# Performance work log

Hardware: AMD Instinct MI355X
Metric: run time of the kernel (lower is better)

The kernel has to match this reference:

```python
import jax, jax.numpy as jnp
import numpy as np

H = 16          # num_heads
K = 15          # kernel_size (padding_l = K-1, causal)
EPS = 1e-5      # LayerNorm eps


def setup_inputs() -> dict:
    key = jax.random.key(0)
    ks = jax.random.split(key, 8)
    T, B, C, F = 1024, 8, 1024, 4096
    n = lambda k, shape, scale=1.0: jax.random.normal(k, shape, jnp.float32) * scale
    return {
        "x": n(ks[0], (T, B, C)),
        "w_lin": n(ks[1], (C, H * K), 0.02),      # dynamic-conv weight projection
        "b_lin": jnp.zeros((H * K,), jnp.float32),
        "ln_g": jnp.ones((C,), jnp.float32),
        "ln_b": jnp.zeros((C,), jnp.float32),
        "fc1_w": n(ks[2], (C, F), 0.02),
        "fc1_b": jnp.zeros((F,), jnp.float32),
        "fc2_w": n(ks[3], (F, C), 0.02),
        "fc2_b": jnp.zeros((C,), jnp.float32),
    }


def _dynamic_conv(x, w_lin, b_lin):
    # x: (T, B, C). Per-timestep weights -> softmax over kernel -> causal conv.
    T, B, C = x.shape
    R = C // H  # channels per head
    w = jnp.einsum('tbc,ck->tbk', x, w_lin) + b_lin          # (T, B, H*K)
    w = jax.nn.softmax(w.reshape(T, B, H, K), axis=-1)        # softmax over kernel taps
    # causal left-padding: tap k sees x[t + k - (K-1)]
    xp = jnp.pad(x, ((K - 1, 0), (0, 0), (0, 0))).reshape(T + K - 1, B, H, R)
    o = jnp.zeros((T, B, H, R), x.dtype)
    for k in range(K):  # fixed small kernel loop; avoids (T,B,C,K) unfold tensor
        o = o + w[:, :, :, k:k + 1] * xp[k:k + T]
    return o.reshape(T, B, C)


def _layer_norm(y, g, b):
    mu = jnp.mean(y, axis=-1, keepdims=True)
    var = jnp.var(y, axis=-1, keepdims=True)
    return (y - mu) * jax.lax.rsqrt(var + EPS) * g + b


def _forward(x, w_lin, b_lin, ln_g, ln_b, fc1_w, fc1_b, fc2_w, fc2_b):
    y = _dynamic_conv(x, w_lin, b_lin)
    y = _layer_norm(y, ln_g, ln_b)
    h = jax.nn.relu(jnp.einsum('tbc,cf->tbf', y, fc1_w) + fc1_b)
    out = jnp.einsum('tbf,fc->tbc', h, fc2_w) + fc2_b
    return out + y  # residual around FFN (residual taken post-LayerNorm)


def reference(x, w_lin, b_lin, ln_g, ln_b, fc1_w, fc1_b, fc2_w, fc2_b):
    return _forward(x, w_lin, b_lin, ln_g, ln_b, fc1_w, fc1_b, fc2_w, fc2_b)
```

## Files before the change

### kernel.cpp

```cpp
#include <hip/hip_runtime.h>


#define T_DIM 1024
#define B_DIM 8
#define C_DIM 1024
#define F_DIM 4096
#define H_DIM 16
#define K_TAP 15
#define TB (T_DIM * B_DIM)

typedef __attribute__((ext_vector_type(8))) short short8;
typedef __attribute__((ext_vector_type(4))) float f32x4;

__device__ __forceinline__ float bf2f(unsigned short u) {
    union { unsigned int i; float f; } v; v.i = ((unsigned int)u) << 16; return v.f;
}
__device__ __forceinline__ unsigned short f2bf(float f) {
    union { float f; unsigned int i; } v; v.f = f;
    unsigned int r = v.i + 0x7fffu + ((v.i >> 16) & 1u);
    return (unsigned short)(r >> 16);
}

__device__ __forceinline__ void async_copy16(const void* gptr, void* lptr) {
    __builtin_amdgcn_global_load_lds(
        (const __attribute__((address_space(1))) void*)gptr,
        (__attribute__((address_space(3))) void*)lptr, 16, 0, 0);
}

__global__ void cvt_bf16(const float* __restrict__ in, unsigned short* __restrict__ out) {
    int i = (blockIdx.x * 256 + threadIdx.x) * 4;
    float4 v = *(const float4*)(in + i);
    unsigned short a = f2bf(v.x), b = f2bf(v.y), c = f2bf(v.z), d = f2bf(v.w);
    uint2 o;
    o.x = (unsigned int)a | ((unsigned int)b << 16);
    o.y = (unsigned int)c | ((unsigned int)d << 16);
    *(uint2*)(out + i) = o;
}

__global__ void transpose_pad(const float* __restrict__ in,
                              unsigned short* __restrict__ out,
                              int R, int Cin, int Cpad) {
    __shared__ unsigned short tile[32][33];
    const int c0 = blockIdx.x * 32, r0 = blockIdx.y * 32;
    const int x = threadIdx.x, y = threadIdx.y;
#pragma unroll
    for (int j = 0; j < 4; j++) {
        int r = r0 + y + j * 8, c = c0 + x;
        unsigned short v = 0;
        if (c < Cin) v = f2bf(in[(size_t)r * Cin + c]);
        tile[y + j * 8][x] = v;
    }
    __syncthreads();
#pragma unroll
    for (int j = 0; j < 4; j++) {
        out[(size_t)(c0 + y + j * 8) * R + (r0 + x)] = tile[x][y + j * 8];
    }
}

template <int MODE>
__global__ __launch_bounds__(256)
void gemm_bt(const unsigned short* __restrict__ A,
             const unsigned short* __restrict__ Bt,
             void* __restrict__ Cout_v,
             int M, int N, int K, int kz,
             const float* __restrict__ bias,
             const unsigned short* __restrict__ resid) {
    __shared__ __align__(16) unsigned short As[2][128 * 32];
    __shared__ __align__(16) unsigned short Bs[2][128 * 32];

    const int tid = threadIdx.x;
    const int m0 = blockIdx.y * 128;
    const int n0 = blockIdx.x * 128;
    const int kbase = blockIdx.z * kz;
    const int wave = tid >> 6, lane = tid & 63;
    const int quad = lane >> 4, l16 = lane & 15;
    const int wm = (wave >> 1) * 64;
    const int wn = (wave & 1) * 64;

    f32x4 acc[4][4];
#pragma unroll
    for (int i = 0; i < 4; i++)
#pragma unroll
        for (int j = 0; j < 4; j++) acc[i][j] = (f32x4){0.f, 0.f, 0.f, 0.f};

    const int r_local = lane >> 2;
    const int kc_g = (lane & 3) ^ ((lane >> 3) & 3);
    const unsigned short* gA0 = A + (size_t)(m0 + wave * 32 + r_local) * K + kbase + kc_g * 8;
    const unsigned short* gA1 = gA0 + (size_t)16 * K;
    const unsigned short* gB0 = Bt + (size_t)(n0 + wave * 32 + r_local) * K + kbase + kc_g * 8;
    const unsigned short* gB1 = gB0 + (size_t)16 * K;
    unsigned short* lA[2] = {&As[0][wave * 32 * 32], &As[1][wave * 32 * 32]};
    unsigned short* lB[2] = {&Bs[0][wave * 32 * 32], &Bs[1][wave * 32 * 32]};

    const int xorsw = (l16 >> 1) & 3;

    async_copy16(gA0, lA[0]);
    async_copy16(gA1, lA[0] + 16 * 32);
    async_copy16(gB0, lB[0]);
    async_copy16(gB1, lB[0] + 16 * 32);

    int buf = 0;
    for (int k0 = 0; k0 < kz; k0 += 32) {
        __syncthreads();

        const int nk = k0 + 32;
        if (nk < kz) {
            const int nb = buf ^ 1;
            async_copy16(gA0 + nk, lA[nb]);
            async_copy16(gA1 + nk, lA[nb] + 16 * 32);
            async_copy16(gB0 + nk, lB[nb]);
            async_copy16(gB1 + nk, lB[nb] + 16 * 32);
        }

        short8 af[4], bfr[4];
#pragma unroll
        for (int i = 0; i < 4; i++) {
            af[i]  = *(const short8*)(&As[buf][(wm + i * 16 + l16) * 32 + (quad ^ xorsw) * 8]);
            bfr[i] = *(const short8*)(&Bs[buf][(wn + i * 16 + l16) * 32 + (quad ^ xorsw) * 8]);
        }
#pragma unroll
        for (int mi = 0; mi < 4; mi++)
#pragma unroll
            for (int nj = 0; nj < 4; nj++)
                acc[mi][nj] = __builtin_amdgcn_mfma_f32_16x16x32_bf16(
                    af[mi], bfr[nj], acc[mi][nj], 0, 0, 0);
        buf ^= 1;
    }

    const int crow0 = m0 + wm + quad * 4;
    const int ccol0 = n0 + wn + l16;
    if (MODE == 3) {
        float* Cf = (float*)Cout_v + (size_t)blockIdx.z * M * N;
#pragma unroll
        for (int mi = 0; mi < 4; mi++)
#pragma unroll
            for (int i = 0; i < 4; i++) {
                int rr = crow0 + mi * 16 + i;
#pragma unroll
                for (int nj = 0; nj < 4; nj++)
                    Cf[(size_t)rr * N + ccol0 + nj * 16] = acc[mi][nj][i];
            }
    } else if (MODE == 1) {
        unsigned short* Cb = (unsigned short*)Cout_v;
        float bv[4];
#pragma unroll
        for (int nj = 0; nj < 4; nj++) bv[nj] = bias[ccol0 + nj * 16];
#pragma unroll
        for (int mi = 0; mi < 4; mi++)
#pragma unroll
            for (int i = 0; i < 4; i++) {
                int rr = crow0 + mi * 16 + i;
#pragma unroll
                for (int nj = 0; nj < 4; nj++) {
                    float v = fmaxf(acc[mi][nj][i] + bv[nj], 0.f);
                    Cb[(size_t)rr * N + ccol0 + nj * 16] = f2bf(v);
                }
            }
    } else {
        float* Cf = (float*)Cout_v;
        float bv[4];
#pragma unroll
        for (int nj = 0; nj < 4; nj++) bv[nj] = bias[ccol0 + nj * 16];
#pragma unroll
        for (int mi = 0; mi < 4; mi++)
#pragma unroll
            for (int i = 0; i < 4; i++) {
                int rr = crow0 + mi * 16 + i;
#pragma unroll
                for (int nj = 0; nj < 4; nj++) {
                    float v = acc[mi][nj][i] + bv[nj]
                            + bf2f(resid[(size_t)rr * N + ccol0 + nj * 16]);
                    Cf[(size_t)rr * N + ccol0 + nj * 16] = v;
                }
            }
    }
}

#define WS_STRIDE ((size_t)TB * 256)
__global__ void softmax_k(const float* __restrict__ wscore,
                          const float* __restrict__ b_lin,
                          float* __restrict__ wconv) {
    int gid = blockIdx.x * 256 + threadIdx.x;
    int row = gid >> 4, hh = gid & 15;
    const float* p = wscore + (size_t)row * 256 + hh * 15;
    float v[K_TAP], mx = -1e30f;
#pragma unroll
    for (int k = 0; k < K_TAP; k++) {
        v[k] = p[k] + p[k + WS_STRIDE] + p[k + 2 * WS_STRIDE] + p[k + 3 * WS_STRIDE]
             + b_lin[hh * K_TAP + k];
        mx = fmaxf(mx, v[k]);
    }
    float s = 0.f;
#pragma unroll
    for (int k = 0; k < K_TAP; k++) { v[k] = __expf(v[k] - mx); s += v[k]; }
    float inv = 1.0f / s;
    float* q = wconv + (size_t)row * 240 + hh * K_TAP;
#pragma unroll
    for (int k = 0; k < K_TAP; k++) q[k] = v[k] * inv;
}

__global__ __launch_bounds__(256)
void conv_ln8(const unsigned short* __restrict__ x,
              const float* __restrict__ wconv,
              const float* __restrict__ ln_g,
              const float* __restrict__ ln_b,
              unsigned short* __restrict__ y) {
    __shared__ __align__(16) unsigned short xs[22][C_DIM];
    __shared__ float wls[8 * 240];
    const int blk = blockIdx.x;
    const int b = blk & 7;
    const int t0 = (blk >> 3) * 8;
    const int tid = threadIdx.x;

#pragma unroll
    for (int k = 0; k < 22; k++) {
        int t = t0 + k - 14;
        uint2 val = make_uint2(0u, 0u);
        if (t >= 0)
            val = *(const uint2*)(x + ((size_t)t * B_DIM + b) * C_DIM + tid * 4);
        *(uint2*)(&xs[k][tid * 4]) = val;
    }
    for (int idx = tid; idx < 8 * 240; idx += 256) {
        int j = idx / 240, o = idx - j * 240;
        wls[idx] = wconv[((size_t)(t0 + j) * B_DIM + b) * 240 + o];
    }
    __syncthreads();

    const int wave = tid >> 6, lane = tid & 63;
    const int ch0 = lane * 16;
    const int h = lane >> 2;

    for (int rj = wave; rj < 8; rj += 4) {
        float acc[16];
#pragma unroll
        for (int i = 0; i < 16; i++) acc[i] = 0.f;
#pragma unroll
        for (int k = 0; k < K_TAP; k++) {
            float w = wls[rj * 240 + h * 15 + k];
            const unsigned short* xr = &xs[rj + k][ch0];
            uint4 p0 = *(const uint4*)(xr);
            uint4 p1 = *(const uint4*)(xr + 8);
            unsigned int uu[8] = {p0.x, p0.y, p0.z, p0.w, p1.x, p1.y, p1.z, p1.w};
#pragma unroll
            for (int q = 0; q < 8; q++) {
                acc[2 * q]     += w * bf2f((unsigned short)(uu[q] & 0xffff));
                acc[2 * q + 1] += w * bf2f((unsigned short)(uu[q] >> 16));
            }
        }
        float s = 0.f, s2 = 0.f;
#pragma unroll
        for (int i = 0; i < 16; i++) { s += acc[i]; s2 += acc[i] * acc[i]; }
#pragma unroll
        for (int off = 32; off > 0; off >>= 1) {
            s  += __shfl_xor(s, off, 64);
            s2 += __shfl_xor(s2, off, 64);
        }
        float mu = s * (1.0f / C_DIM);
        float var = s2 * (1.0f / C_DIM) - mu * mu;
        float rs = rsqrtf(var + 1e-5f);

        unsigned short o16[16];
#pragma unroll
        for (int i = 0; i < 16; i++)
            o16[i] = f2bf((acc[i] - mu) * rs * ln_g[ch0 + i] + ln_b[ch0 + i]);
        uint4 w0, w1;
        w0.x = (unsigned int)o16[0]  | ((unsigned int)o16[1]  << 16);
        w0.y = (unsigned int)o16[2]  | ((unsigned int)o16[3]  << 16);
        w0.z = (unsigned int)o16[4]  | ((unsigned int)o16[5]  << 16);
        w0.w = (unsigned int)o16[6]  | ((unsigned int)o16[7]  << 16);
        w1.x = (unsigned int)o16[8]  | ((unsigned int)o16[9]  << 16);
        w1.y = (unsigned int)o16[10] | ((unsigned int)o16[11] << 16);
        w1.z = (unsigned int)o16[12] | ((unsigned int)o16[13] << 16);
        w1.w = (unsigned int)o16[14] | ((unsigned int)o16[15] << 16);
        unsigned short* yr = y + ((size_t)(t0 + rj) * B_DIM + b) * C_DIM + ch0;
        *(uint4*)(yr) = w0;
        *(uint4*)(yr + 8) = w1;
    }
}

extern "C" void kernel_launch(void* const* d_in, const int* in_sizes, int n_in,
                              void* d_out, int out_size, void* d_ws, size_t ws_size,
                              hipStream_t stream) {
    const float* x     = (const float*)d_in[0];
    const float* w_lin = (const float*)d_in[1];
    const float* b_lin = (const float*)d_in[2];
    const float* ln_g  = (const float*)d_in[3];
    const float* ln_b  = (const float*)d_in[4];
    const float* fc1_w = (const float*)d_in[5];
    const float* fc1_b = (const float*)d_in[6];
    const float* fc2_w = (const float*)d_in[7];
    const float* fc2_b = (const float*)d_in[8];
    float* out = (float*)d_out;

    char* ws = (char*)d_ws;
    unsigned short* xb    = (unsigned short*)(ws);
    unsigned short* fc1T  = (unsigned short*)(ws + 16777216);
    unsigned short* fc2T  = (unsigned short*)(ws + 25165824);
    unsigned short* wlinT = (unsigned short*)(ws + 33554432);
    unsigned short* y     = (unsigned short*)(ws + 34078720);
    unsigned short* h     = (unsigned short*)(ws + 50855936);
    float* wscore = (float*)(ws + 50855936);
    float* wconv  = (float*)(ws + 50855936 + 33554432);

    cvt_bf16<<<TB * C_DIM / 1024, 256, 0, stream>>>(x, xb);

    dim3 tb(32, 8);
    transpose_pad<<<dim3(F_DIM / 32, C_DIM / 32), tb, 0, stream>>>(fc1_w, fc1T, C_DIM, F_DIM, F_DIM);
    transpose_pad<<<dim3(C_DIM / 32, F_DIM / 32), tb, 0, stream>>>(fc2_w, fc2T, F_DIM, C_DIM, C_DIM);
    transpose_pad<<<dim3(256 / 32, C_DIM / 32), tb, 0, stream>>>(w_lin, wlinT, C_DIM, 240, 256);

    gemm_bt<3><<<dim3(256 / 128, TB / 128, 4), 256, 0, stream>>>(
        xb, wlinT, (void*)wscore, TB, 256, C_DIM, C_DIM / 4, nullptr, nullptr);

    softmax_k<<<TB * H_DIM / 256, 256, 0, stream>>>(wscore, b_lin, wconv);

    conv_ln8<<<TB / 8, 256, 0, stream>>>(xb, wconv, ln_g, ln_b, y);

    gemm_bt<1><<<dim3(F_DIM / 128, TB / 128, 1), 256, 0, stream>>>(
        y, fc1T, (void*)h, TB, F_DIM, C_DIM, C_DIM, fc1_b, nullptr);

    gemm_bt<2><<<dim3(C_DIM / 128, TB / 128, 1), 256, 0, stream>>>(
        h, fc2T, (void*)out, TB, C_DIM, F_DIM, F_DIM, fc2_b, y);
}
```

Baseline: 356.6 us.

## Deepen GEMM K-tile to 64, merge prep kernels, fuse softmax into conv

The GEMM K-step grows from 32 to 64, with 8-chunk XOR swizzled LDS, so each barrier covers twice as many MFMAs. The separate convert and transpose kernels become one launch, and the softmax runs inside the conv/LayerNorm kernel, dropping a launch and the wconv round trip through memory. The fc2 GEMM grid is swapped so consecutive blocks walk M. LDS use doubles to 64KB per block, which may reduce occupancy.

```diff
diff --git a/kernel.cpp b/kernel.cpp
--- a/kernel.cpp
+++ b/kernel.cpp
@@ -27,37 +27,53 @@
         (__attribute__((address_space(3))) void*)lptr, 16, 0, 0);
 }
 
-__global__ void cvt_bf16(const float* __restrict__ in, unsigned short* __restrict__ out) {
-    int i = (blockIdx.x * 256 + threadIdx.x) * 4;
-    float4 v = *(const float4*)(in + i);
-    unsigned short a = f2bf(v.x), b = f2bf(v.y), c = f2bf(v.z), d = f2bf(v.w);
-    uint2 o;
-    o.x = (unsigned int)a | ((unsigned int)b << 16);
-    o.y = (unsigned int)c | ((unsigned int)d << 16);
-    *(uint2*)(out + i) = o;
-}
-
-__global__ void transpose_pad(const float* __restrict__ in,
-                              unsigned short* __restrict__ out,
-                              int R, int Cin, int Cpad) {
+__global__ __launch_bounds__(256)
+void prep(const float* __restrict__ x, unsigned short* __restrict__ xb,
+          const float* __restrict__ fc1_w, unsigned short* __restrict__ fc1T,
+          const float* __restrict__ fc2_w, unsigned short* __restrict__ fc2T,
+          const float* __restrict__ w_lin, unsigned short* __restrict__ wlinT) {
+    const int bid = blockIdx.x;
+    const int tid = threadIdx.x;
+    if (bid < 8192) {
+        int i = (bid * 256 + tid) * 4;
+        float4 v = *(const float4*)(x + i);
+        uint2 o;
+        o.x = (unsigned int)f2bf(v.x) | ((unsigned int)f2bf(v.y) << 16);
+        o.y = (unsigned int)f2bf(v.z) | ((unsigned int)f2bf(v.w) << 16);
+        *(uint2*)(xb + i) = o;
+        return;
+    }
+    const float* in; unsigned short* out; int R, Cin, c0, r0;
+    if (bid < 12288) {
+        int idx = bid - 8192;
+        in = fc1_w; out = fc1T; R = C_DIM; Cin = F_DIM;
+        c0 = (idx & 127) * 32; r0 = (idx >> 7) * 32;
+    } else if (bid < 16384) {
+        int idx = bid - 12288;
+        in = fc2_w; out = fc2T; R = F_DIM; Cin = C_DIM;
+        c0 = (idx & 31) * 32; r0 = (idx >> 5) * 32;
+    } else {
+        int idx = bid - 16384;
+        in = w_lin; out = wlinT; R = C_DIM; Cin = 240;
+        c0 = (idx & 7) * 32; r0 = (idx >> 3) * 32;
+    }
     __shared__ unsigned short tile[32][33];
-    const int c0 = blockIdx.x * 32, r0 = blockIdx.y * 32;
-    const int x = threadIdx.x, y = threadIdx.y;
+    const int xx = tid & 31, yy = tid >> 5;
 #pragma unroll
     for (int j = 0; j < 4; j++) {
-        int r = r0 + y + j * 8, c = c0 + x;
+        int r = r0 + yy + j * 8, c = c0 + xx;
         unsigned short v = 0;
         if (c < Cin) v = f2bf(in[(size_t)r * Cin + c]);
-        tile[y + j * 8][x] = v;
+        tile[yy + j * 8][xx] = v;
     }
     __syncthreads();
 #pragma unroll
     for (int j = 0; j < 4; j++) {
-        out[(size_t)(c0 + y + j * 8) * R + (r0 + x)] = tile[x][y + j * 8];
-    }
-}
-
-template <int MODE>
+        out[(size_t)(c0 + yy + j * 8) * R + (r0 + xx)] = tile[xx][yy + j * 8];
+    }
+}
+
+template <int MODE, int SWAP>
 __global__ __launch_bounds__(256)
 void gemm_bt(const unsigned short* __restrict__ A,
              const unsigned short* __restrict__ Bt,
@@ -65,12 +81,12 @@
              int M, int N, int K, int kz,
              const float* __restrict__ bias,
              const unsigned short* __restrict__ resid) {
-    __shared__ __align__(16) unsigned short As[2][128 * 32];
-    __shared__ __align__(16) unsigned short Bs[2][128 * 32];
+    __shared__ __align__(16) unsigned short As[2][128 * 64];
+    __shared__ __align__(16) unsigned short Bs[2][128 * 64];
 
     const int tid = threadIdx.x;
-    const int m0 = blockIdx.y * 128;
-    const int n0 = blockIdx.x * 128;
+    const int m0 = (SWAP ? blockIdx.x : blockIdx.y) * 128;
+    const int n0 = (SWAP ? blockIdx.y : blockIdx.x) * 128;
     const int kbase = blockIdx.z * kz;
     const int wave = tid >> 6, lane = tid & 63;
     const int quad = lane >> 4, l16 = lane & 15;
@@ -83,47 +99,52 @@
 #pragma unroll
         for (int j = 0; j < 4; j++) acc[i][j] = (f32x4){0.f, 0.f, 0.f, 0.f};
 
-    const int r_local = lane >> 2;
-    const int kc_g = (lane & 3) ^ ((lane >> 3) & 3);
-    const unsigned short* gA0 = A + (size_t)(m0 + wave * 32 + r_local) * K + kbase + kc_g * 8;
-    const unsigned short* gA1 = gA0 + (size_t)16 * K;
-    const unsigned short* gB0 = Bt + (size_t)(n0 + wave * 32 + r_local) * K + kbase + kc_g * 8;
-    const unsigned short* gB1 = gB0 + (size_t)16 * K;
-    unsigned short* lA[2] = {&As[0][wave * 32 * 32], &As[1][wave * 32 * 32]};
-    unsigned short* lB[2] = {&Bs[0][wave * 32 * 32], &Bs[1][wave * 32 * 32]};
-
-    const int xorsw = (l16 >> 1) & 3;
-
-    async_copy16(gA0, lA[0]);
-    async_copy16(gA1, lA[0] + 16 * 32);
-    async_copy16(gB0, lB[0]);
-    async_copy16(gB1, lB[0] + 16 * 32);
-
+    const int rsub = lane >> 3;
+    const int gch = (lane & 7) ^ rsub;
+    const unsigned short* gA = A + (size_t)(m0 + wave * 32 + rsub) * K + kbase + gch * 8;
+    const unsigned short* gB = Bt + (size_t)(n0 + wave * 32 + rsub) * K + kbase + gch * 8;
+    unsigned short* lA[2] = {&As[0][wave * 32 * 64], &As[1][wave * 32 * 64]};
+    unsigned short* lB[2] = {&Bs[0][wave * 32 * 64], &Bs[1][wave * 32 * 64]};
+
+#pragma unroll
+    for (int j = 0; j < 4; j++) {
+        async_copy16(gA + (size_t)j * 8 * K, lA[0] + j * 8 * 64);
+        async_copy16(gB + (size_t)j * 8 * K, lB[0] + j * 8 * 64);
+    }
+
+    const int swz = l16 & 7;
     int buf = 0;
-    for (int k0 = 0; k0 < kz; k0 += 32) {
+    for (int k0 = 0; k0 < kz; k0 += 64) {
         __syncthreads();
 
-        const int nk = k0 + 32;
+        const int nk = k0 + 64;
         if (nk < kz) {
             const int nb = buf ^ 1;
-            async_copy16(gA0 + nk, lA[nb]);
-            async_copy16(gA1 + nk, lA[nb] + 16 * 32);
-            async_copy16(gB0 + nk, lB[nb]);
-            async_copy16(gB1 + nk, lB[nb] + 16 * 32);
-        }
-
-        short8 af[4], bfr[4];
-#pragma unroll
-        for (int i = 0; i < 4; i++) {
-            af[i]  = *(const short8*)(&As[buf][(wm + i * 16 + l16) * 32 + (quad ^ xorsw) * 8]);
-            bfr[i] = *(const short8*)(&Bs[buf][(wn + i * 16 + l16) * 32 + (quad ^ xorsw) * 8]);
-        }
-#pragma unroll
-        for (int mi = 0; mi < 4; mi++)
-#pragma unroll
-            for (int nj = 0; nj < 4; nj++)
-                acc[mi][nj] = __builtin_amdgcn_mfma_f32_16x16x32_bf16(
-                    af[mi], bfr[nj], acc[mi][nj], 0, 0, 0);
+#pragma unroll
+            for (int j = 0; j < 4; j++) {
+                async_copy16(gA + nk + (size_t)j * 8 * K, lA[nb] + j * 8 * 64);
+                async_copy16(gB + nk + (size_t)j * 8 * K, lB[nb] + j * 8 * 64);
+            }
+        }
+
+        short8 af[2][4], bfr[2][4];
+#pragma unroll
+        for (int kk = 0; kk < 2; kk++) {
+            const int c = kk * 4 + quad;
+#pragma unroll
+            for (int i = 0; i < 4; i++) {
+                af[kk][i]  = *(const short8*)(&As[buf][(wm + i * 16 + l16) * 64 + (c ^ swz) * 8]);
+                bfr[kk][i] = *(const short8*)(&Bs[buf][(wn + i * 16 + l16) * 64 + (c ^ swz) * 8]);
+            }
+        }
+#pragma unroll
+        for (int kk = 0; kk < 2; kk++)
+#pragma unroll
+            for (int mi = 0; mi < 4; mi++)
+#pragma unroll
+                for (int nj = 0; nj < 4; nj++)
+                    acc[mi][nj] = __builtin_amdgcn_mfma_f32_16x16x32_bf16(
+                        af[kk][mi], bfr[kk][nj], acc[mi][nj], 0, 0, 0);
         buf ^= 1;
     }
 
@@ -177,34 +198,13 @@
 }
 
 #define WS_STRIDE ((size_t)TB * 256)
-__global__ void softmax_k(const float* __restrict__ wscore,
-                          const float* __restrict__ b_lin,
-                          float* __restrict__ wconv) {
-    int gid = blockIdx.x * 256 + threadIdx.x;
-    int row = gid >> 4, hh = gid & 15;
-    const float* p = wscore + (size_t)row * 256 + hh * 15;
-    float v[K_TAP], mx = -1e30f;
-#pragma unroll
-    for (int k = 0; k < K_TAP; k++) {
-        v[k] = p[k] + p[k + WS_STRIDE] + p[k + 2 * WS_STRIDE] + p[k + 3 * WS_STRIDE]
-             + b_lin[hh * K_TAP + k];
-        mx = fmaxf(mx, v[k]);
-    }
-    float s = 0.f;
-#pragma unroll
-    for (int k = 0; k < K_TAP; k++) { v[k] = __expf(v[k] - mx); s += v[k]; }
-    float inv = 1.0f / s;
-    float* q = wconv + (size_t)row * 240 + hh * K_TAP;
-#pragma unroll
-    for (int k = 0; k < K_TAP; k++) q[k] = v[k] * inv;
-}
-
 __global__ __launch_bounds__(256)
-void conv_ln8(const unsigned short* __restrict__ x,
-              const float* __restrict__ wconv,
-              const float* __restrict__ ln_g,
-              const float* __restrict__ ln_b,
-              unsigned short* __restrict__ y) {
+void conv_ln8s(const unsigned short* __restrict__ x,
+               const float* __restrict__ wscore,
+               const float* __restrict__ b_lin,
+               const float* __restrict__ ln_g,
+               const float* __restrict__ ln_b,
+               unsigned short* __restrict__ y) {
     __shared__ __align__(16) unsigned short xs[22][C_DIM];
     __shared__ float wls[8 * 240];
     const int blk = blockIdx.x;
@@ -212,6 +212,25 @@
     const int t0 = (blk >> 3) * 8;
     const int tid = threadIdx.x;
 
+    if (tid < 128) {
+        const int rj = tid >> 4, hh = tid & 15;
+        const size_t row = (size_t)(t0 + rj) * B_DIM + b;
+        const float* p = wscore + row * 256 + hh * 15;
+        float v[K_TAP], mx = -1e30f;
+#pragma unroll
+        for (int k = 0; k < K_TAP; k++) {
+            v[k] = p[k] + p[k + WS_STRIDE] + p[k + 2 * WS_STRIDE] + p[k + 3 * WS_STRIDE]
+                 + b_lin[hh * K_TAP + k];
+            mx = fmaxf(mx, v[k]);
+        }
+        float s = 0.f;
+#pragma unroll
+        for (int k = 0; k < K_TAP; k++) { v[k] = __expf(v[k] - mx); s += v[k]; }
+        float inv = 1.0f / s;
+#pragma unroll
+        for (int k = 0; k < K_TAP; k++) wls[rj * 240 + hh * K_TAP + k] = v[k] * inv;
+    }
+
 #pragma unroll
     for (int k = 0; k < 22; k++) {
         int t = t0 + k - 14;
@@ -219,10 +238,6 @@
         if (t >= 0)
             val = *(const uint2*)(x + ((size_t)t * B_DIM + b) * C_DIM + tid * 4);
         *(uint2*)(&xs[k][tid * 4]) = val;
-    }
-    for (int idx = tid; idx < 8 * 240; idx += 256) {
-        int j = idx / 240, o = idx - j * 240;
-        wls[idx] = wconv[((size_t)(t0 + j) * B_DIM + b) * 240 + o];
     }
     __syncthreads();
 
@@ -300,25 +315,17 @@
     unsigned short* y     = (unsigned short*)(ws + 34078720);
     unsigned short* h     = (unsigned short*)(ws + 50855936);
     float* wscore = (float*)(ws + 50855936);
-    float* wconv  = (float*)(ws + 50855936 + 33554432);
-
-    cvt_bf16<<<TB * C_DIM / 1024, 256, 0, stream>>>(x, xb);
-
-    dim3 tb(32, 8);
-    transpose_pad<<<dim3(F_DIM / 32, C_DIM / 32), tb, 0, stream>>>(fc1_w, fc1T, C_DIM, F_DIM, F_DIM);
-    transpose_pad<<<dim3(C_DIM / 32, F_DIM / 32), tb, 0, stream>>>(fc2_w, fc2T, F_DIM, C_DIM, C_DIM);
-    transpose_pad<<<dim3(256 / 32, C_DIM / 32), tb, 0, stream>>>(w_lin, wlinT, C_DIM, 240, 256);
-
-    gemm_bt<3><<<dim3(256 / 128, TB / 128, 4), 256, 0, stream>>>(
+
+    prep<<<16640, 256, 0, stream>>>(x, xb, fc1_w, fc1T, fc2_w, fc2T, w_lin, wlinT);
+
+    gemm_bt<3, 0><<<dim3(256 / 128, TB / 128, 4), 256, 0, stream>>>(
         xb, wlinT, (void*)wscore, TB, 256, C_DIM, C_DIM / 4, nullptr, nullptr);
 
-    softmax_k<<<TB * H_DIM / 256, 256, 0, stream>>>(wscore, b_lin, wconv);
-
-    conv_ln8<<<TB / 8, 256, 0, stream>>>(xb, wconv, ln_g, ln_b, y);
-
-    gemm_bt<1><<<dim3(F_DIM / 128, TB / 128, 1), 256, 0, stream>>>(
+    conv_ln8s<<<TB / 8, 256, 0, stream>>>(xb, wscore, b_lin, ln_g, ln_b, y);
+
+    gemm_bt<1, 0><<<dim3(F_DIM / 128, TB / 128, 1), 256, 0, stream>>>(
         y, fc1T, (void*)h, TB, F_DIM, C_DIM, C_DIM, fc1_b, nullptr);
 
-    gemm_bt<2><<<dim3(C_DIM / 128, TB / 128, 1), 256, 0, stream>>>(
+    gemm_bt<2, 1><<<dim3(TB / 128, C_DIM / 128, 1), 256, 0, stream>>>(
         h, fc2T, (void*)out, TB, C_DIM, F_DIM, F_DIM, fc2_b, y);
 }
```

New measurement: 316.0 us. -11.4%, faster.
